# Kernel tuning notes

Measured on AMD Instinct MI355X. Metric: run time of the kernel, lower is better.

Reference implementation:

```python
import jax, jax.numpy as jnp
import numpy as np

N, D_IN, D_HID, D_OUT, E = 8192, 1024, 4096, 1024, 8
N_ACTIVE = max(1, int(E * 0.625))  # 5
TEMP = float(np.e)               # temperature = np.e in source


def setup_inputs() -> dict:
    key = jax.random.key(0)
    ks = jax.random.split(key, 4)
    return {
        "x": jax.random.normal(ks[0], (N, D_IN), jnp.float32),
        "gate_w": jax.random.normal(ks[1], (D_IN, E), jnp.float32) * 0.02,
        "gate_b": jnp.zeros((E,), jnp.float32),
        "w1": jax.random.normal(ks[2], (E, D_IN, D_HID), jnp.float32) * 0.02,
        "b1": jnp.zeros((E, D_HID), jnp.float32),
        "w2": jax.random.normal(ks[3], (E, D_HID, D_OUT), jnp.float32) * 0.02,
        "b2": jnp.zeros((E, D_OUT), jnp.float32),
    }


def reference(x, gate_w, gate_b, w1, b1, w2, b2):
    # Gate: softmax over experts at temperature e, then top-k mask + renormalize
    scores = (x @ gate_w + gate_b) / TEMP                 # [N, E]
    probs = jax.nn.softmax(scores, axis=-1)               # [N, E]
    _, topk_idx = jax.lax.top_k(probs, N_ACTIVE)          # [N, k]
    mask = jax.nn.one_hot(topk_idx, E, dtype=probs.dtype).sum(axis=-2)  # [N, E]
    weights = probs * mask
    weights = weights / (weights.sum(axis=-1, keepdims=True) + 1e-8)
    # Dense all-experts FFN (dropout is eval-mode identity)
    h = jax.nn.relu(jnp.einsum('nd,edh->neh', x, w1) + b1)   # [N, E, d_hid]
    e_out = jnp.einsum('neh,eho->neo', h, w2) + b2           # [N, E, d_out]
    # Camp A (first E/2 experts) added, camp G subtracted: out = out_a - out_g
    sign = jnp.where(jnp.arange(E) < E // 2, 1.0, -1.0)      # [E]
    return jnp.einsum('ne,neo->no', weights * sign, e_out)   # [N, d_out]
```

## Files before the change

kernel.cpp:

```cpp
#include <hip/hip_runtime.h>
#include <hip/hip_bf16.h>
#include <cmath>


typedef _Float16 f16;
typedef _Float16 f16x8 __attribute__((ext_vector_type(8)));
typedef _Float16 f16x4 __attribute__((ext_vector_type(4)));
typedef float f32x4 __attribute__((ext_vector_type(4)));

#define NROWS 8192
#define DIN   1024
#define DHID  4096
#define DOUT  1024
#define NEXP  8

#define OFF_SGATE 0u
#define OFF_XH    262144u
#define OFF_W1T   17039360u
#define OFF_W2T   84148224u
#define OFF_P1    151257088u
#define OFF_HH    184811520u
#define NEED_NE1  251920384ull
#define NEED_NE2  319029248ull
#define NEED_NE4  453246976ull
#define NEED_NE8  721682432ull

__device__ __forceinline__ void gload_lds16(const void* gsrc, void* ldsdst) {
  __builtin_amdgcn_global_load_lds(
      (const __attribute__((address_space(1))) unsigned int*)gsrc,
      (__attribute__((address_space(3))) unsigned int*)ldsdst, 16, 0, 0);
}

__global__ void gate_kernel(const float* __restrict__ x,
                            const float* __restrict__ gw,
                            const float* __restrict__ gb,
                            float* __restrict__ sgate) {
  const int row = blockIdx.x * 4 + (threadIdx.x >> 6);
  const int l = threadIdx.x & 63;
  const float* xr = x + (size_t)row * DIN;
  float acc[8] = {0.f,0.f,0.f,0.f,0.f,0.f,0.f,0.f};
#pragma unroll
  for (int j = 0; j < 16; ++j) {
    const int k = l + 64 * j;
    const float xv = xr[k];
    const float4 g0 = *(const float4*)(gw + (size_t)k * 8);
    const float4 g1 = *(const float4*)(gw + (size_t)k * 8 + 4);
    acc[0] += xv * g0.x; acc[1] += xv * g0.y; acc[2] += xv * g0.z; acc[3] += xv * g0.w;
    acc[4] += xv * g1.x; acc[5] += xv * g1.y; acc[6] += xv * g1.z; acc[7] += xv * g1.w;
  }
#pragma unroll
  for (int off = 32; off > 0; off >>= 1) {
#pragma unroll
    for (int e = 0; e < 8; ++e) acc[e] += __shfl_xor(acc[e], off, 64);
  }
  if (l == 0) {
    const float invT = 0.36787944117144233f;
    float p[8]; float mx = -1e30f;
#pragma unroll
    for (int e = 0; e < 8; ++e) { p[e] = (acc[e] + gb[e]) * invT; mx = fmaxf(mx, p[e]); }
    float S = 0.f;
#pragma unroll
    for (int e = 0; e < 8; ++e) { p[e] = expf(p[e] - mx); S += p[e]; }
    const float inv = 1.0f / S;
#pragma unroll
    for (int e = 0; e < 8; ++e) p[e] *= inv;
    bool keep[8] = {true,true,true,true,true,true,true,true};
    for (int t = 0; t < 3; ++t) {
      float pmin = 1e30f; int mi = -1;
      for (int e = 0; e < 8; ++e)
        if (keep[e] && (p[e] < pmin || (p[e] == pmin && e > mi))) { pmin = p[e]; mi = e; }
      keep[mi] = false;
    }
    float wsum = 0.f;
#pragma unroll
    for (int e = 0; e < 8; ++e) if (keep[e]) wsum += p[e];
    const float rinv = 1.0f / (wsum + 1e-8f);
#pragma unroll
    for (int e = 0; e < 8; ++e) {
      const float wv = keep[e] ? p[e] * rinv : 0.0f;
      sgate[(size_t)row * 8 + e] = (e < 4) ? wv : -wv;
    }
  }
}

__global__ void cvt_x_kernel(const float* __restrict__ x, f16* __restrict__ xh) {
  const size_t i = ((size_t)blockIdx.x * blockDim.x + threadIdx.x) * 4;
  const float4 v = *(const float4*)(x + i);
  f16x4 o = { (f16)v.x, (f16)v.y, (f16)v.z, (f16)v.w };
  *(f16x4*)(xh + i) = o;
}

__global__ void transpose_cvt(const float* __restrict__ in, f16* __restrict__ out,
                              int R, int C) {
  __shared__ float tile[32][33];
  const int e = blockIdx.z;
  const float* ine = in + (size_t)e * R * C;
  f16* oute = out + (size_t)e * R * C;
  const int c0 = blockIdx.x * 32, r0 = blockIdx.y * 32;
  const int tx = threadIdx.x, ty = threadIdx.y;
#pragma unroll
  for (int i = 0; i < 4; ++i)
    tile[ty + i * 8][tx] = ine[(size_t)(r0 + ty + i * 8) * C + c0 + tx];
  __syncthreads();
#pragma unroll
  for (int i = 0; i < 4; ++i)
    oute[(size_t)(c0 + ty + i * 8) * R + r0 + tx] = (f16)tile[tx][ty + i * 8];
}

#define MFMAOP(a_, b_, c_) __builtin_amdgcn_mfma_f32_16x16x32_f16(a_, b_, c_, 0, 0, 0)

template <int EPI>
__global__ __launch_bounds__(512, 2) void gemm8p(
    const f16* __restrict__ A, int lda,
    const f16* __restrict__ B, int ldb, int nt,
    long long khA, long long khB,
    const float* __restrict__ bias,
    f16* __restrict__ outH, int ldc,
    float* outP0, float* outP1, int p1w,
    const float* __restrict__ sgate, int expert, int gx) {
  __shared__ alignas(16) f16 lA[4 * 8192];
  __shared__ alignas(16) f16 lB[4 * 8192];
  const int tid = threadIdx.x;
  const int l = tid & 63, w = tid >> 6;
  const int wr = w >> 2, wc = w & 3;

  const int nwg = gridDim.x, cpx = nwg >> 3;
  const int lg = ((int)blockIdx.x & 7) * cpx + ((int)blockIdx.x >> 3);

  int m0, n0;
  const f16* Aeff = A;
  const f16* Beff = B;
  float* P = nullptr;
  bool pw = false;
  if constexpr (EPI == 1) {
    m0 = (lg / gx) * 256; n0 = (lg % gx) * 256;
  } else {
    const int xx = lg >> 5, cc = lg & 31;
    const int kh = xx >> 2;
    n0 = (xx & 3) * 256;
    m0 = cc * 256;
    Aeff = A + (size_t)kh * (size_t)khA;
    Beff = B + (size_t)kh * (size_t)khB;
    P = kh ? outP1 : outP0;
    pw = (p1w != 0);
  }

  const int srow = tid >> 2;
  const int sxc = (tid & 3) ^ ((tid >> 3) & 3);
  const f16* pA = Aeff + (size_t)(m0 + srow) * lda + sxc * 8;
  const f16* pB = Beff + (size_t)(n0 + srow) * ldb + sxc * 8;

  auto BOFS = [&](int tk) -> size_t {
    if constexpr (EPI == 1) return (size_t)tk * 32;
    else return (size_t)(tk >> 7) * (size_t)(DOUT * DHID) +
                (size_t)(tk & 127) * 32;
  };

#define STG_A(S, H, TK) \
    gload_lds16(pA + (size_t)(H) * 128 * lda + (size_t)(TK) * 32, \
                lA + (S) * 8192 + (H) * 4096 + w * 512)
#define STG_B(S, H, TK) \
    gload_lds16(pB + (size_t)(H) * 128 * ldb + BOFS(TK), \
                lB + (S) * 8192 + (H) * 4096 + w * 512)

  int aofs[8], bofs4[4];
  {
    const int cg = l >> 4;
#pragma unroll
    for (int f = 0; f < 8; ++f) {
      const int r = wr * 128 + f * 16 + (l & 15);
      aofs[f] = r * 64 + ((cg ^ ((r >> 1) & 3)) << 4);
    }
#pragma unroll
    for (int g = 0; g < 4; ++g) {
      const int r = wc * 64 + g * 16 + (l & 15);
      bofs4[g] = r * 64 + ((cg ^ ((r >> 1) & 3)) << 4);
    }
  }
#define RA(S, f) (*(const f16x8*)((const char*)lA + (S) * 16384 + aofs[f]))
#define RB(S, g) (*(const f16x8*)((const char*)lB + (S) * 16384 + bofs4[g]))

#define SYNC() do { __builtin_amdgcn_s_barrier(); \
    asm volatile("s_waitcnt lgkmcnt(0)" ::: "memory"); \
    __builtin_amdgcn_sched_barrier(0); } while (0)
#define ENDPH() do { __builtin_amdgcn_s_setprio(0); \
    __builtin_amdgcn_s_barrier(); } while (0)
#define VM8() do { asm volatile("s_waitcnt vmcnt(8)" ::: "memory"); \
    __builtin_amdgcn_sched_barrier(0); } while (0)
#define VM4() do { asm volatile("s_waitcnt vmcnt(4)" ::: "memory"); \
    __builtin_amdgcn_sched_barrier(0); } while (0)
#define VM0() do { asm volatile("s_waitcnt vmcnt(0)" ::: "memory"); \
    __builtin_amdgcn_sched_barrier(0); } while (0)
#define MM(f, g, ar, br) acc[f][g] = MFMAOP(ar, br, acc[f][g])

  f32x4 acc[8][4] = {};
  f16x8 fa0, fa1, fa2, fa3;
  f16x8 fb0, fb1, fb2, fb3;

#define BODY(T, S, S3) do { \
     \
    fa0 = RA(S, 0); fa1 = RA(S, 1); fa2 = RA(S, 2); fa3 = RA(S, 3); \
    fb0 = RB(S, 0); fb1 = RB(S, 1); fb2 = RB(S, 2); fb3 = RB(S, 3); \
    if ((T) + 3 < nt) { STG_A(S3, 0, (T) + 3); STG_A(S3, 1, (T) + 3); } \
    SYNC(); \
    __builtin_amdgcn_s_setprio(1); \
    MM(0,0,fa0,fb0); MM(0,1,fa0,fb1); MM(0,2,fa0,fb2); MM(0,3,fa0,fb3); \
    MM(1,0,fa1,fb0); MM(1,1,fa1,fb1); MM(1,2,fa1,fb2); MM(1,3,fa1,fb3); \
    MM(2,0,fa2,fb0); MM(2,1,fa2,fb1); MM(2,2,fa2,fb2); MM(2,3,fa2,fb3); \
    MM(3,0,fa3,fb0); MM(3,1,fa3,fb1); MM(3,2,fa3,fb2); MM(3,3,fa3,fb3); \
    ENDPH(); \
     \
    fa0 = RA(S, 4); fa1 = RA(S, 5); fa2 = RA(S, 6); fa3 = RA(S, 7); \
    if ((T) + 3 < nt) { STG_B(S3, 0, (T) + 3); STG_B(S3, 1, (T) + 3); } \
    if ((T) + 3 < nt) VM8(); else if ((T) + 2 < nt) VM4(); else VM0(); \
    SYNC(); \
    __builtin_amdgcn_s_setprio(1); \
    MM(4,0,fa0,fb0); MM(4,1,fa0,fb1); MM(4,2,fa0,fb2); MM(4,3,fa0,fb3); \
    MM(5,0,fa1,fb0); MM(5,1,fa1,fb1); MM(5,2,fa1,fb2); MM(5,3,fa1,fb3); \
    MM(6,0,fa2,fb0); MM(6,1,fa2,fb1); MM(6,2,fa2,fb2); MM(6,3,fa2,fb3); \
    MM(7,0,fa3,fb0); MM(7,1,fa3,fb1); MM(7,2,fa3,fb2); MM(7,3,fa3,fb3); \
    ENDPH(); \
  } while (0)

  STG_A(0, 0, 0); STG_A(0, 1, 0); STG_B(0, 0, 0); STG_B(0, 1, 0);
  STG_A(1, 0, 1); STG_A(1, 1, 1); STG_B(1, 0, 1); STG_B(1, 1, 1);
  STG_A(2, 0, 2); STG_A(2, 1, 2); STG_B(2, 0, 2); STG_B(2, 1, 2);
  VM8();
  __builtin_amdgcn_s_barrier();

  for (int T = 0; T < nt; T += 4) {
    BODY(T + 0, 0, 3);
    BODY(T + 1, 1, 0);
    BODY(T + 2, 2, 1);
    BODY(T + 3, 3, 2);
  }
  asm volatile("s_waitcnt vmcnt(0)" ::: "memory");

  if constexpr (EPI == 1) {
#pragma unroll
    for (int mi = 0; mi < 8; ++mi)
#pragma unroll
      for (int r = 0; r < 4; ++r) {
        const int row = m0 + wr * 128 + mi * 16 + (l >> 4) * 4 + r;
        const float sg = sgate[(size_t)row * 8 + expert];
#pragma unroll
        for (int ni = 0; ni < 4; ++ni) {
          const int col = n0 + wc * 64 + ni * 16 + (l & 15);
          const float v = acc[mi][ni][r] + bias[col];
          outH[(size_t)row * ldc + col] = (f16)(fmaxf(v, 0.0f) * sg);
        }
      }
  } else {
    float* const scr = (w < 4) ? (float*)lA + w * 4096
                               : (float*)lB + (w - 4) * 4096;
    const int hl = l >> 4, ll = l & 15;
#pragma unroll
    for (int p = 0; p < 2; ++p) {
#pragma unroll
      for (int mi4 = 0; mi4 < 4; ++mi4)
#pragma unroll
        for (int r = 0; r < 4; ++r) {
          const int rowl = mi4 * 16 + hl * 4 + r;
#pragma unroll
          for (int ni = 0; ni < 4; ++ni)
            scr[rowl * 64 + ni * 16 + ll] = acc[p * 4 + mi4][ni][r];
        }
#pragma unroll
      for (int i = 0; i < 16; ++i) {
        const int rowl = hl + i * 4;
        f32x4 v = *(const f32x4*)(scr + rowl * 64 + ll * 4);
        const int row = m0 + wr * 128 + p * 64 + rowl;
        const int col = n0 + wc * 64 + ll * 4;
        f32x4* gp = (f32x4*)(P + (size_t)row * 1024 + col);
        if (!pw) {
          const f32x4 g = *gp;
          v[0] += g[0]; v[1] += g[1]; v[2] += g[2]; v[3] += g[3];
        }
        *gp = v;
      }
    }
  }
#undef STG_A
#undef STG_B
#undef RA
#undef RB
#undef SYNC
#undef ENDPH
#undef VM8
#undef VM4
#undef VM0
#undef MM
#undef BODY
}

template <bool WITHP>
__global__ void finalize_out(const float* p0,
                             const float* __restrict__ p1,
                             const float* __restrict__ sgate,
                             const float* __restrict__ b2,
                             float* out) {
  const int i = blockIdx.x * 256 + threadIdx.x;
  const int n = i >> 8, c4 = i & 255;
  float4 a = make_float4(0.f, 0.f, 0.f, 0.f);
  if constexpr (WITHP) {
    const float4 u = ((const float4*)p0)[i];
    const float4 v = ((const float4*)p1)[i];
    a.x = u.x + v.x; a.y = u.y + v.y; a.z = u.z + v.z; a.w = u.w + v.w;
  }
  const float* sg = sgate + (size_t)n * 8;
#pragma unroll
  for (int e = 0; e < 8; ++e) {
    const float s = sg[e];
    const float4 bv = ((const float4*)(b2 + (size_t)e * 1024))[c4];
    a.x += s * bv.x; a.y += s * bv.y; a.z += s * bv.z; a.w += s * bv.w;
  }
  ((float4*)out)[i] = a;
}

extern "C" void kernel_launch(void* const* d_in, const int* in_sizes, int n_in,
                              void* d_out, int out_size, void* d_ws, size_t ws_size,
                              hipStream_t stream) {
  const float* x  = (const float*)d_in[0];
  const float* gw = (const float*)d_in[1];
  const float* gb = (const float*)d_in[2];
  const float* w1 = (const float*)d_in[3];
  const float* b1 = (const float*)d_in[4];
  const float* w2 = (const float*)d_in[5];
  const float* b2 = (const float*)d_in[6];
  float* out = (float*)d_out;

  char* ws = (char*)d_ws;
  float* sgate = (float*)(ws + OFF_SGATE);
  f16* xh  = (f16*)(ws + OFF_XH);
  f16* w1t = (f16*)(ws + OFF_W1T);
  f16* w2t = (f16*)(ws + OFF_W2T);
  float* p1 = (float*)(ws + OFF_P1);
  f16* hh  = (f16*)(ws + OFF_HH);

  const int NE = (ws_size >= NEED_NE8) ? 8 :
                 (ws_size >= NEED_NE4) ? 4 :
                 (ws_size >= NEED_NE2) ? 2 : 1;

  gate_kernel<<<NROWS / 4, 256, 0, stream>>>(x, gw, gb, sgate);
  cvt_x_kernel<<<(NROWS * DIN) / (256 * 4), 256, 0, stream>>>(x, xh);
  transpose_cvt<<<dim3(DHID / 32, DIN / 32, NEXP), dim3(32, 8), 0, stream>>>(w1, w1t, DIN, DHID);
  transpose_cvt<<<dim3(DOUT / 32, DHID / 32, NEXP), dim3(32, 8), 0, stream>>>(w2, w2t, DHID, DOUT);

  const int ngrp = NEXP / NE;
  const long long khB = (NE == 1) ? 2048LL : (long long)(NE / 2) * DOUT * DHID;
  for (int g = 0; g < ngrp; ++g) {
    for (int ei = 0; ei < NE; ++ei) {
      const int e = g * NE + ei;
      gemm8p<1><<<512, 512, 0, stream>>>(
          xh, DIN, w1t + (size_t)e * DHID * DIN, DIN, DIN / 32,
          0, 0,
          b1 + (size_t)e * DHID, hh + (size_t)ei * DHID, NE * DHID,
          nullptr, nullptr, 0, sgate, e, DHID / 256);
    }
    gemm8p<2><<<256, 512, 0, stream>>>(
        hh, NE * DHID, w2t + (size_t)g * NE * DOUT * DHID, DHID, NE * 64,
        (long long)NE * 2048, khB,
        nullptr, nullptr, 0, out, p1, (g == 0) ? 1 : 0, nullptr, 0, 0);
  }
  finalize_out<true><<<(NROWS * DOUT) / (256 * 4), 256, 0, stream>>>(
      out, p1, sgate, b2, out);
}
```

Measured before the change: 1.633 ms.

## Double K-tile depth to 64 in GEMM pipeline and cap expert grouping at two

```diff
diff --git a/kernel.cpp b/kernel.cpp
--- a/kernel.cpp
+++ b/kernel.cpp
@@ -20,10 +20,7 @@
 #define OFF_W2T   84148224u
 #define OFF_P1    151257088u
 #define OFF_HH    184811520u
-#define NEED_NE1  251920384ull
 #define NEED_NE2  319029248ull
-#define NEED_NE4  453246976ull
-#define NEED_NE8  721682432ull
 
 __device__ __forceinline__ void gload_lds16(const void* gsrc, void* ldsdst) {
   __builtin_amdgcn_global_load_lds(
@@ -145,49 +142,38 @@
     pw = (p1w != 0);
   }
 
-  const int srow = tid >> 2;
-  const int sxc = (tid & 3) ^ ((tid >> 3) & 3);
+  const int srow = tid >> 3;
+  const int sxc = (tid & 7) ^ (srow & 7);
   const f16* pA = Aeff + (size_t)(m0 + srow) * lda + sxc * 8;
   const f16* pB = Beff + (size_t)(n0 + srow) * ldb + sxc * 8;
-
-  auto BOFS = [&](int tk) -> size_t {
-    if constexpr (EPI == 1) return (size_t)tk * 32;
-    else return (size_t)(tk >> 7) * (size_t)(DOUT * DHID) +
-                (size_t)(tk & 127) * 32;
-  };
-
-#define STG_A(S, H, TK) \
-    gload_lds16(pA + (size_t)(H) * 128 * lda + (size_t)(TK) * 32, \
-                lA + (S) * 8192 + (H) * 4096 + w * 512)
-#define STG_B(S, H, TK) \
-    gload_lds16(pB + (size_t)(H) * 128 * ldb + BOFS(TK), \
-                lB + (S) * 8192 + (H) * 4096 + w * 512)
-
-  int aofs[8], bofs4[4];
-  {
-    const int cg = l >> 4;
-#pragma unroll
-    for (int f = 0; f < 8; ++f) {
-      const int r = wr * 128 + f * 16 + (l & 15);
-      aofs[f] = r * 64 + ((cg ^ ((r >> 1) & 3)) << 4);
-    }
-#pragma unroll
-    for (int g = 0; g < 4; ++g) {
-      const int r = wc * 64 + g * 16 + (l & 15);
-      bofs4[g] = r * 64 + ((cg ^ ((r >> 1) & 3)) << 4);
-    }
-  }
-#define RA(S, f) (*(const f16x8*)((const char*)lA + (S) * 16384 + aofs[f]))
-#define RB(S, g) (*(const f16x8*)((const char*)lB + (S) * 16384 + bofs4[g]))
-
+  f16* const dA = lA + w * 512;
+  f16* const dB = lB + w * 512;
+
+#define STG_A(slot, h, tk) do { \
+    const f16* s_ = pA + (size_t)(h) * 128 * lda + (size_t)(tk) * 64; \
+    gload_lds16(s_,            dA + (slot) * 8192); \
+    gload_lds16(s_ + 64 * lda, dA + (slot) * 8192 + 4096); \
+  } while (0)
+#define STG_B(slot, h, tk) do { \
+    const f16* s_ = pB + (size_t)(h) * 128 * ldb + (size_t)(tk) * 64; \
+    gload_lds16(s_,            dB + (slot) * 8192); \
+    gload_lds16(s_ + 64 * ldb, dB + (slot) * 8192 + 4096); \
+  } while (0)
+
+  const int cg = l >> 4, xr = l & 7;
+  const int ok0 = ((cg ^ xr) << 4);
+  const int ok1 = (((4 + cg) ^ xr) << 4);
+  const char* const baA = (const char*)lA + (l & 15) * 128;
+  const char* const baB = (const char*)lB + (wc & 1) * 8192 + (l & 15) * 128;
+
+#define RDA(CA, f, o) (*(const f16x8*)(baA + ((CA) + wr) * 16384 + (f) * 2048 + (o)))
+#define RDB(CB, g, o) (*(const f16x8*)(baB + ((CB) + (wc >> 1)) * 16384 + (g) * 2048 + (o)))
 #define SYNC() do { __builtin_amdgcn_s_barrier(); \
     asm volatile("s_waitcnt lgkmcnt(0)" ::: "memory"); \
     __builtin_amdgcn_sched_barrier(0); } while (0)
 #define ENDPH() do { __builtin_amdgcn_s_setprio(0); \
     __builtin_amdgcn_s_barrier(); } while (0)
-#define VM8() do { asm volatile("s_waitcnt vmcnt(8)" ::: "memory"); \
-    __builtin_amdgcn_sched_barrier(0); } while (0)
-#define VM4() do { asm volatile("s_waitcnt vmcnt(4)" ::: "memory"); \
+#define VM6() do { asm volatile("s_waitcnt vmcnt(6)" ::: "memory"); \
     __builtin_amdgcn_sched_barrier(0); } while (0)
 #define VM0() do { asm volatile("s_waitcnt vmcnt(0)" ::: "memory"); \
     __builtin_amdgcn_sched_barrier(0); } while (0)
@@ -195,44 +181,70 @@
 
   f32x4 acc[8][4] = {};
   f16x8 fa0, fa1, fa2, fa3;
-  f16x8 fb0, fb1, fb2, fb3;
-
-#define BODY(T, S, S3) do { \
+  f16x8 ga0, ga1, ga2, ga3;
+  f16x8 b00, b10, b20, b30;
+  f16x8 b01, b11, b21, b31;
+
+#define TILEBODY(T, CA, CB, SB1, SB0n, SA0n, SA1n) do { \
      \
-    fa0 = RA(S, 0); fa1 = RA(S, 1); fa2 = RA(S, 2); fa3 = RA(S, 3); \
-    fb0 = RB(S, 0); fb1 = RB(S, 1); fb2 = RB(S, 2); fb3 = RB(S, 3); \
-    if ((T) + 3 < nt) { STG_A(S3, 0, (T) + 3); STG_A(S3, 1, (T) + 3); } \
+    fa0 = RDA(CA, 0, ok0); fa1 = RDA(CA, 1, ok0); \
+    fa2 = RDA(CA, 2, ok0); fa3 = RDA(CA, 3, ok0); \
+    b00 = RDB(CB, 0, ok0); b10 = RDB(CB, 1, ok0); \
+    b20 = RDB(CB, 2, ok0); b30 = RDB(CB, 3, ok0); \
+    if ((T) + 1 < nt) STG_B(SB1, 1, (T) + 1); \
     SYNC(); \
     __builtin_amdgcn_s_setprio(1); \
-    MM(0,0,fa0,fb0); MM(0,1,fa0,fb1); MM(0,2,fa0,fb2); MM(0,3,fa0,fb3); \
-    MM(1,0,fa1,fb0); MM(1,1,fa1,fb1); MM(1,2,fa1,fb2); MM(1,3,fa1,fb3); \
-    MM(2,0,fa2,fb0); MM(2,1,fa2,fb1); MM(2,2,fa2,fb2); MM(2,3,fa2,fb3); \
-    MM(3,0,fa3,fb0); MM(3,1,fa3,fb1); MM(3,2,fa3,fb2); MM(3,3,fa3,fb3); \
+    MM(0,0,fa0,b00); MM(0,1,fa0,b10); MM(0,2,fa0,b20); MM(0,3,fa0,b30); \
+    MM(1,0,fa1,b00); MM(1,1,fa1,b10); MM(1,2,fa1,b20); MM(1,3,fa1,b30); \
+    MM(2,0,fa2,b00); MM(2,1,fa2,b10); MM(2,2,fa2,b20); MM(2,3,fa2,b30); \
+    MM(3,0,fa3,b00); MM(3,1,fa3,b10); MM(3,2,fa3,b20); MM(3,3,fa3,b30); \
     ENDPH(); \
      \
-    fa0 = RA(S, 4); fa1 = RA(S, 5); fa2 = RA(S, 6); fa3 = RA(S, 7); \
-    if ((T) + 3 < nt) { STG_B(S3, 0, (T) + 3); STG_B(S3, 1, (T) + 3); } \
-    if ((T) + 3 < nt) VM8(); else if ((T) + 2 < nt) VM4(); else VM0(); \
+    ga0 = RDA(CA, 0, ok1); ga1 = RDA(CA, 1, ok1); \
+    ga2 = RDA(CA, 2, ok1); ga3 = RDA(CA, 3, ok1); \
+    b01 = RDB(CB, 0, ok1); b11 = RDB(CB, 1, ok1); \
+    b21 = RDB(CB, 2, ok1); b31 = RDB(CB, 3, ok1); \
     SYNC(); \
     __builtin_amdgcn_s_setprio(1); \
-    MM(4,0,fa0,fb0); MM(4,1,fa0,fb1); MM(4,2,fa0,fb2); MM(4,3,fa0,fb3); \
-    MM(5,0,fa1,fb0); MM(5,1,fa1,fb1); MM(5,2,fa1,fb2); MM(5,3,fa1,fb3); \
-    MM(6,0,fa2,fb0); MM(6,1,fa2,fb1); MM(6,2,fa2,fb2); MM(6,3,fa2,fb3); \
-    MM(7,0,fa3,fb0); MM(7,1,fa3,fb1); MM(7,2,fa3,fb2); MM(7,3,fa3,fb3); \
+    MM(0,0,ga0,b01); MM(0,1,ga0,b11); MM(0,2,ga0,b21); MM(0,3,ga0,b31); \
+    MM(1,0,ga1,b01); MM(1,1,ga1,b11); MM(1,2,ga1,b21); MM(1,3,ga1,b31); \
+    MM(2,0,ga2,b01); MM(2,1,ga2,b11); MM(2,2,ga2,b21); MM(2,3,ga2,b31); \
+    MM(3,0,ga3,b01); MM(3,1,ga3,b11); MM(3,2,ga3,b21); MM(3,3,ga3,b31); \
+    ENDPH(); \
+     \
+    fa0 = RDA(CA, 4, ok0); fa1 = RDA(CA, 5, ok0); \
+    fa2 = RDA(CA, 6, ok0); fa3 = RDA(CA, 7, ok0); \
+    ga0 = RDA(CA, 4, ok1); ga1 = RDA(CA, 5, ok1); \
+    ga2 = RDA(CA, 6, ok1); ga3 = RDA(CA, 7, ok1); \
+    if ((T) + 2 < nt) STG_B(SB0n, 0, (T) + 2); \
+    SYNC(); \
+    __builtin_amdgcn_s_setprio(1); \
+    MM(4,0,fa0,b00); MM(4,1,fa0,b10); MM(4,2,fa0,b20); MM(4,3,fa0,b30); \
+    MM(5,0,fa1,b00); MM(5,1,fa1,b10); MM(5,2,fa1,b20); MM(5,3,fa1,b30); \
+    MM(6,0,fa2,b00); MM(6,1,fa2,b10); MM(6,2,fa2,b20); MM(6,3,fa2,b30); \
+    MM(7,0,fa3,b00); MM(7,1,fa3,b10); MM(7,2,fa3,b20); MM(7,3,fa3,b30); \
+    ENDPH(); \
+     \
+    if ((T) + 2 < nt) { STG_A(SA0n, 0, (T) + 2); STG_A(SA1n, 1, (T) + 2); \
+                        VM6(); } \
+    else { VM0(); } \
+    SYNC(); \
+    __builtin_amdgcn_s_setprio(1); \
+    MM(4,0,ga0,b01); MM(4,1,ga0,b11); MM(4,2,ga0,b21); MM(4,3,ga0,b31); \
+    MM(5,0,ga1,b01); MM(5,1,ga1,b11); MM(5,2,ga1,b21); MM(5,3,ga1,b31); \
+    MM(6,0,ga2,b01); MM(6,1,ga2,b11); MM(6,2,ga2,b21); MM(6,3,ga2,b31); \
+    MM(7,0,ga3,b01); MM(7,1,ga3,b11); MM(7,2,ga3,b21); MM(7,3,ga3,b31); \
     ENDPH(); \
   } while (0)
 
-  STG_A(0, 0, 0); STG_A(0, 1, 0); STG_B(0, 0, 0); STG_B(0, 1, 0);
-  STG_A(1, 0, 1); STG_A(1, 1, 1); STG_B(1, 0, 1); STG_B(1, 1, 1);
-  STG_A(2, 0, 2); STG_A(2, 1, 2); STG_B(2, 0, 2); STG_B(2, 1, 2);
-  VM8();
+  STG_A(0, 0, 0); STG_B(0, 0, 0); STG_A(1, 1, 0); STG_B(1, 1, 0);
+  STG_A(2, 0, 1); STG_B(2, 0, 1); STG_A(3, 1, 1);
+  asm volatile("s_waitcnt vmcnt(6)" ::: "memory");
   __builtin_amdgcn_s_barrier();
 
-  for (int T = 0; T < nt; T += 4) {
-    BODY(T + 0, 0, 3);
-    BODY(T + 1, 1, 0);
-    BODY(T + 2, 2, 1);
-    BODY(T + 3, 3, 2);
+  for (int t = 0; t < nt; t += 2) {
+    TILEBODY(t,     0, 0, 3, 0, 0, 1);
+    TILEBODY(t + 1, 2, 2, 1, 2, 2, 3);
   }
   asm volatile("s_waitcnt vmcnt(0)" ::: "memory");
 
@@ -282,15 +294,14 @@
   }
 #undef STG_A
 #undef STG_B
-#undef RA
-#undef RB
+#undef RDA
+#undef RDB
 #undef SYNC
 #undef ENDPH
-#undef VM8
-#undef VM4
+#undef VM6
 #undef VM0
 #undef MM
-#undef BODY
+#undef TILEBODY
 }
 
 template <bool WITHP>
@@ -337,29 +348,30 @@
   float* p1 = (float*)(ws + OFF_P1);
   f16* hh  = (f16*)(ws + OFF_HH);
 
-  const int NE = (ws_size >= NEED_NE8) ? 8 :
-                 (ws_size >= NEED_NE4) ? 4 :
-                 (ws_size >= NEED_NE2) ? 2 : 1;
+  const int NE = (ws_size >= NEED_NE2) ? 2 : 1;
+  const int ngrp = NEXP / NE;
 
   gate_kernel<<<NROWS / 4, 256, 0, stream>>>(x, gw, gb, sgate);
   cvt_x_kernel<<<(NROWS * DIN) / (256 * 4), 256, 0, stream>>>(x, xh);
   transpose_cvt<<<dim3(DHID / 32, DIN / 32, NEXP), dim3(32, 8), 0, stream>>>(w1, w1t, DIN, DHID);
   transpose_cvt<<<dim3(DOUT / 32, DHID / 32, NEXP), dim3(32, 8), 0, stream>>>(w2, w2t, DHID, DOUT);
 
-  const int ngrp = NEXP / NE;
-  const long long khB = (NE == 1) ? 2048LL : (long long)(NE / 2) * DOUT * DHID;
+  const long long khA = (long long)NE * 2048;
+  const long long khB = (NE == 2) ? (long long)DOUT * DHID
+                                  : 2048LL;
+  const int nt2 = NE * 32;
   for (int g = 0; g < ngrp; ++g) {
     for (int ei = 0; ei < NE; ++ei) {
       const int e = g * NE + ei;
       gemm8p<1><<<512, 512, 0, stream>>>(
-          xh, DIN, w1t + (size_t)e * DHID * DIN, DIN, DIN / 32,
+          xh, DIN, w1t + (size_t)e * DHID * DIN, DIN, DIN / 64,
           0, 0,
           b1 + (size_t)e * DHID, hh + (size_t)ei * DHID, NE * DHID,
           nullptr, nullptr, 0, sgate, e, DHID / 256);
     }
     gemm8p<2><<<256, 512, 0, stream>>>(
-        hh, NE * DHID, w2t + (size_t)g * NE * DOUT * DHID, DHID, NE * 64,
-        (long long)NE * 2048, khB,
+        hh, NE * DHID, w2t + (size_t)g * NE * DOUT * DHID, DHID, nt2,
+        khA, khB,
         nullptr, nullptr, 0, out, p1, (g == 0) ? 1 : 0, nullptr, 0, 0);
   }
   finalize_out<true><<<(NROWS * DOUT) / (256 * 4), 256, 0, stream>>>(
```

Measured after the change: 1.428 ms. -12.5%, faster.
